# Kernel optimization log

Measured on AMD Instinct MI355X. Metric: run time of the kernel, lower is better.

## Reference

```python
import jax, jax.numpy as jnp
import numpy as np

B, S, E, H = 4, 2048, 1024, 16
HD = E // H  # 64 head dim


def setup_inputs() -> dict:
    key = jax.random.key(0)
    ks = jax.random.split(key, 6)
    x = jax.random.normal(ks[0], (B, S, E), dtype=jnp.float32)
    mask = jax.random.randint(ks[1], (B, S, S), 0, 2, dtype=jnp.int32)
    # per-head qkv Linear(E -> 3*HD), stacked over heads: weight [H, 3*HD, E]
    lim = 1.0 / np.sqrt(E)
    Wqkv = jax.random.uniform(ks[2], (H, 3 * HD, E), minval=-lim, maxval=lim, dtype=jnp.float32)
    bqkv = jax.random.uniform(ks[3], (H, 3 * HD), minval=-lim, maxval=lim, dtype=jnp.float32)
    Wo = jax.random.uniform(ks[4], (E, E), minval=-lim, maxval=lim, dtype=jnp.float32)
    bo = jax.random.uniform(ks[5], (E,), minval=-lim, maxval=lim, dtype=jnp.float32)
    return {"x": x, "mask": mask, "Wqkv": Wqkv, "bqkv": bqkv, "Wo": Wo, "bo": bo}


def reference(x, mask, Wqkv, bqkv, Wo, bo):
    # fused per-head qkv projection: [B,S,E] x [H,3HD,E] -> [B,H,S,3HD]
    qkv = jnp.einsum('bse,hfe->bhsf', x, Wqkv) + bqkv[None, :, None, :]
    q, k, v = jnp.split(qkv, 3, axis=-1)  # each [B,H,S,HD]
    scale = 1.0 / jnp.sqrt(jnp.float32(HD))
    scores = jnp.einsum('bhqd,bhkd->bhqk', q, k) * scale  # [B,H,S,S]
    # NOTE: original masked_fill sets masked scores to 0.0 (not -inf)
    scores = jnp.where(mask[:, None, :, :] == 1, 0.0, scores)
    attn = jax.nn.softmax(scores, axis=-1)
    ctx = jnp.einsum('bhqk,bhkd->bhqd', attn, v)  # [B,H,S,HD]
    ctx = ctx.transpose(0, 2, 1, 3).reshape(B, S, E)  # concat heads
    return ctx @ Wo.T + bo
```

## Files before the change

kernel.cpp:

```cpp
#include <hip/hip_runtime.h>
#include <stdint.h>

#define B_ 4
#define S_ 2048
#define E_ 1024
#define H_ 16
#define HD_ 64

typedef __attribute__((ext_vector_type(8))) short bf16x8;
typedef __attribute__((ext_vector_type(4))) float f32x4;

__device__ __forceinline__ ushort f2b(float f) {
    union { float f; uint32_t u; } c; c.f = f;
    return (ushort)((c.u + 0x8000u) >> 16);
}

__device__ __forceinline__ uint32_t pkbf(float a, float b) {
    union { float f; uint32_t u; } ca, cb; ca.f = a; cb.f = b;
#if __has_builtin(__builtin_amdgcn_perm)
    return __builtin_amdgcn_perm(cb.u + 0x8000u, ca.u + 0x8000u, 0x07060302u);
#else
    return (uint32_t)f2b(a) | ((uint32_t)f2b(b) << 16);
#endif
}

#if __has_builtin(__builtin_amdgcn_exp2f)
#define EXP2(x) __builtin_amdgcn_exp2f(x)
#else
#define EXP2(x) exp2f(x)
#endif

__device__ __forceinline__ void gl2lds16(const ushort* g, const ushort* l) {
    __builtin_amdgcn_global_load_lds(
        (const __attribute__((address_space(1))) unsigned int*)g,
        (__attribute__((address_space(3))) unsigned int*)l,
        16, 0, 0);
}

__global__ __launch_bounds__(256) void cvt_all(
    const float* __restrict__ x, const float* __restrict__ wq, const float* __restrict__ wo,
    ushort* __restrict__ xb, ushort* __restrict__ wqb, ushort* __restrict__ wob) {
    int i = blockIdx.x * 256 + threadIdx.x;
    const float* src; ushort* dst; int off;
    if (i < 2097152)      { src = x;  dst = xb;  off = i; }
    else if (i < 2883584) { src = wq; dst = wqb; off = i - 2097152; }
    else                  { src = wo; dst = wob; off = i - 2883584; }
    float4 f = ((const float4*)src)[off];
    ushort4 o;
    o.x = f2b(f.x); o.y = f2b(f.y); o.z = f2b(f.z); o.w = f2b(f.w);
    ((ushort4*)dst)[off] = o;
}

__global__ __launch_bounds__(256) void pack_mask(const int* __restrict__ mask,
                                                 uint32_t* __restrict__ mb) {
    int i = blockIdx.x * 256 + threadIdx.x;
    unsigned long long bal = __ballot(mask[i] == 1);
    int lane = threadIdx.x & 63;
    if (lane < 2) {
        int b = i >> 22, q = (i >> 11) & 2047, c = i & 2047;
        int kt = c >> 6;
        mb[((uint64_t)(b * 32 + kt) * 2048 + q) * 2 + lane] =
            (lane == 0) ? (uint32_t)bal : (uint32_t)(bal >> 32);
    }
}

template <int KD>
__device__ __forceinline__ void gemm_bt_core(
    const ushort* __restrict__ A, const ushort* __restrict__ Bm,
    int m0, int n0, ushort* As, ushort* Bs, f32x4 (&acc)[4][4])
{
    const int tid  = threadIdx.x;
    const int lane = tid & 63;
    const int wave = tid >> 6;
    const int wm = wave >> 1, wn = wave & 1;
    const int fr = lane & 15;
    const int fk = (lane >> 4) * 8;
    const int lrow = lane >> 2;
    const int lk   = (lane & 3) * 8;

    const f32x4 fz = {0.f, 0.f, 0.f, 0.f};
#pragma unroll
    for (int i = 0; i < 4; ++i)
#pragma unroll
        for (int j = 0; j < 4; ++j) acc[i][j] = fz;

    for (int kt = 0; kt < KD / 32; ++kt) {
        const int k0 = kt * 32;
        __syncthreads();
#pragma unroll
        for (int t = 0; t < 2; ++t) {
            const int r0 = t * 64 + wave * 16;
            gl2lds16(&A [(uint64_t)(m0 + r0 + lrow) * KD + k0 + lk], &As[r0 * 32]);
            gl2lds16(&Bm[(uint64_t)(n0 + r0 + lrow) * KD + k0 + lk], &Bs[r0 * 32]);
        }
        __syncthreads();
        bf16x8 af[4], bfr[4];
#pragma unroll
        for (int i = 0; i < 4; ++i)
            af[i] = *(const bf16x8*)&As[(wm * 64 + i * 16 + fr) * 32 + fk];
#pragma unroll
        for (int j = 0; j < 4; ++j)
            bfr[j] = *(const bf16x8*)&Bs[(wn * 64 + j * 16 + fr) * 32 + fk];
#pragma unroll
        for (int i = 0; i < 4; ++i)
#pragma unroll
            for (int j = 0; j < 4; ++j)
                acc[i][j] = __builtin_amdgcn_mfma_f32_16x16x32_bf16(af[i], bfr[j], acc[i][j], 0, 0, 0);
    }
}

__global__ __launch_bounds__(256) void qkv_gemm(
    const ushort* __restrict__ xb, const ushort* __restrict__ wb,
    const float* __restrict__ bqkv,
    ushort* __restrict__ qo, ushort* __restrict__ ko, ushort* __restrict__ vto)
{
    __shared__ ushort As[128 * 32];
    __shared__ ushort Bs[128 * 32];
    f32x4 acc[4][4];
    const int m0 = blockIdx.x * 128;
    const int n0 = blockIdx.y * 128;
    gemm_bt_core<1024>(xb, wb, m0, n0, As, Bs, acc);

    const int lane = threadIdx.x & 63, wave = threadIdx.x >> 6;
    const int wm = wave >> 1, wn = wave & 1;
    const int col = lane & 15, rg = lane >> 4;
    const float QSC = 0.125f * 1.4426950408889634f;
#pragma unroll
    for (int j = 0; j < 4; ++j) {
        const int n = n0 + wn * 64 + j * 16 + col;
        const int h = n / 192, f = n % 192;
        const float bias = bqkv[n];
#pragma unroll
        for (int i2 = 0; i2 < 4; ++i2) {
            const int mbase = m0 + wm * 64 + i2 * 16 + rg * 4;
            if (f < 128) {
#pragma unroll
                for (int v = 0; v < 4; ++v) {
                    const int m = mbase + v;
                    const int b = m >> 11, s = m & 2047;
                    const float val = acc[i2][j][v] + bias;
                    if (f < 64) qo[((uint64_t)(b * 16 + h) * 2048 + s) * 64 + f]        = f2b(val * QSC);
                    else        ko[((uint64_t)(b * 16 + h) * 2048 + s) * 64 + (f - 64)] = f2b(val);
                }
            } else {
                const int b = mbase >> 11, s = mbase & 2047;
                ushort4 pk;
                pk.x = f2b(acc[i2][j][0] + bias);
                pk.y = f2b(acc[i2][j][1] + bias);
                pk.z = f2b(acc[i2][j][2] + bias);
                pk.w = f2b(acc[i2][j][3] + bias);
                *(ushort4*)&vto[((uint64_t)(b * 16 + h) * 64 + (f - 128)) * 2048 + s] = pk;
            }
        }
    }
}

__global__ __launch_bounds__(256, 4) void attn_kernel(
    const ushort* __restrict__ qa, const ushort* __restrict__ ka,
    const ushort* __restrict__ vta, const uint32_t* __restrict__ mbits,
    ushort* __restrict__ ctxo)
{
    __shared__ __align__(16) ushort LDSH[16384];
    ushort* const Ks0 = LDSH;
    ushort* const Vt0 = LDSH + 4096;
    ushort* const Ks1 = LDSH + 8192;
    ushort* const Vt1 = LDSH + 12288;
    ushort* const CTX = LDSH + 8192;

    const int bid = blockIdx.x;
    const int bh = (bid & 7) * 8 + (bid >> 7);
    const int qb = (bid >> 3) & 15;
    const int b = bh >> 4;
    const int tid = threadIdx.x, lane = tid & 63, wave = tid >> 6;
    const int col = lane & 15, rg = lane >> 4;

    const uint64_t bhoff = (uint64_t)bh * (S_ * 64);
    const ushort* qp = qa + bhoff + (uint64_t)qb * 128 * 64;
    const ushort* kp = ka + bhoff;
    const ushort* vp = vta + bhoff;
    const uint32_t* mk0 = mbits + ((uint64_t)(b * 32) * 2048 + qb * 128 + wave * 32 + col) * 2;
    const uint32_t* mk1 = mk0 + 32;

    const int lr = lane >> 3;
    const int usw = (lane & 7) ^ lr;
    const int r0s = wave * 16 + lr;
    const int r1s = r0s + 8;
    const int sg0 = (r0s & 32) | ((r0s & 12) << 1) | ((r0s & 16) >> 2) | (r0s & 3);
    const int sg1 = (r1s & 32) | ((r1s & 12) << 1) | ((r1s & 16) >> 2) | (r1s & 3);
    const int kb0 = sg0 * 64 + usw * 8;
    const int kb1 = sg1 * 64 + usw * 8;
    const int vb0 = r0s * 2048 + usw * 8;
    const int vb1 = r1s * 2048 + usw * 8;
    const int ldst0 = wave * 1024;
    const int ldst1 = ldst0 + 512;

    bf16x8 aq[2][2];
#pragma unroll
    for (int i = 0; i < 2; ++i)
#pragma unroll
        for (int k2 = 0; k2 < 2; ++k2)
            aq[i][k2] = *(const bf16x8*)&qp[(wave * 32 + i * 16 + col) * 64 + k2 * 32 + rg * 8];

    gl2lds16(&kp[kb0], &Ks0[ldst0]);
    gl2lds16(&kp[kb1], &Ks0[ldst1]);
    gl2lds16(&vp[vb0], &Vt0[ldst0]);
    gl2lds16(&vp[vb1], &Vt0[ldst1]);
    uint2 mc0 = *(const uint2*)mk0;
    uint2 mc1 = *(const uint2*)mk1;
    uint2 mn0 = mc0, mn1 = mc1;
    __syncthreads();

    const f32x4 fz = {0.f, 0.f, 0.f, 0.f};
    f32x4 acc[4][2];
#pragma unroll
    for (int dt = 0; dt < 4; ++dt)
#pragma unroll
        for (int i = 0; i < 2; ++i) acc[dt][i] = fz;
    f32x4 acc5[2] = {fz, fz};

    bf16x8 vone;
#pragma unroll
    for (int e = 0; e < 8; ++e) vone[e] = (short)0x3F80;

    uint32_t bsel[2][4];
#pragma unroll
    for (int p = 0; p < 2; ++p)
#pragma unroll
        for (int v = 0; v < 4; ++v) bsel[p][v] = 1u << (rg * 8 + p * 4 + v);

    const int u0 = (rg ^ (col & 7)) << 3;

#pragma unroll 2
    for (int kt = 0; kt < 32; ++kt) {
        const int buf = kt & 1;
        const ushort* const Ksb = buf ? Ks1 : Ks0;
        const ushort* const Vtb = buf ? Vt1 : Vt0;
        ushort* const Ksn = buf ? Ks0 : Ks1;
        ushort* const Vtn = buf ? Vt0 : Vt1;

        if (kt < 31) {
            const int knext = (kt + 1) * 4096;
            gl2lds16(&kp[knext + kb0], &Ksn[ldst0]);
            gl2lds16(&kp[knext + kb1], &Ksn[ldst1]);
            gl2lds16(&vp[vb0 + (kt + 1) * 64], &Vtn[ldst0]);
            gl2lds16(&vp[vb1 + (kt + 1) * 64], &Vtn[ldst1]);
            mn0 = *(const uint2*)(mk0 + (uint64_t)(kt + 1) * 4096);
            mn1 = *(const uint2*)(mk1 + (uint64_t)(kt + 1) * 4096);
        }

        f32x4 sc[2][4];
        __builtin_amdgcn_s_setprio(1);
#pragma unroll
        for (int j = 0; j < 4; ++j) {
            bf16x8 bk0 = *(const bf16x8*)&Ksb[(j * 16 + col) * 64 + u0];
            bf16x8 bk1 = *(const bf16x8*)&Ksb[(j * 16 + col) * 64 + (u0 ^ 32)];
#pragma unroll
            for (int i = 0; i < 2; ++i) {
                f32x4 z = __builtin_amdgcn_mfma_f32_16x16x32_bf16(bk0, aq[i][0], fz, 0, 0, 0);
                sc[i][j] = __builtin_amdgcn_mfma_f32_16x16x32_bf16(bk1, aq[i][1], z, 0, 0, 0);
            }
        }
        __builtin_amdgcn_s_setprio(0);

        bf16x8 bp[2][2];
#pragma unroll
        for (int i = 0; i < 2; ++i) {
            const uint2 mw = i ? mc1 : mc0;
            union { uint32_t w[4]; bf16x8 v; } p0, p1;
#pragma unroll
            for (int j = 0; j < 4; ++j) {
                const uint32_t w = (j & 2) ? mw.y : mw.x;
                const int p = j & 1;
                float pe[4];
#pragma unroll
                for (int v = 0; v < 4; ++v) {
                    const float s = (w & bsel[p][v]) ? 0.f : sc[i][j][v];
                    pe[v] = EXP2(s);
                }
                const uint32_t lo = pkbf(pe[0], pe[1]);
                const uint32_t hi = pkbf(pe[2], pe[3]);
                if (j < 2) { p0.w[p * 2] = lo; p0.w[p * 2 + 1] = hi; }
                else       { p1.w[p * 2] = lo; p1.w[p * 2 + 1] = hi; }
            }
            bp[i][0] = p0.v;
            bp[i][1] = p1.v;
        }

        __builtin_amdgcn_s_setprio(1);
#pragma unroll
        for (int i = 0; i < 2; ++i) {
            acc5[i] = __builtin_amdgcn_mfma_f32_16x16x32_bf16(vone, bp[i][0], acc5[i], 0, 0, 0);
            acc5[i] = __builtin_amdgcn_mfma_f32_16x16x32_bf16(vone, bp[i][1], acc5[i], 0, 0, 0);
        }
#pragma unroll
        for (int dt = 0; dt < 4; ++dt) {
            bf16x8 av0 = *(const bf16x8*)&Vtb[(dt * 16 + col) * 64 + u0];
            bf16x8 av1 = *(const bf16x8*)&Vtb[(dt * 16 + col) * 64 + (u0 ^ 32)];
#pragma unroll
            for (int i = 0; i < 2; ++i) {
                acc[dt][i] = __builtin_amdgcn_mfma_f32_16x16x32_bf16(av0, bp[i][0], acc[dt][i], 0, 0, 0);
                acc[dt][i] = __builtin_amdgcn_mfma_f32_16x16x32_bf16(av1, bp[i][1], acc[dt][i], 0, 0, 0);
            }
        }
        __builtin_amdgcn_s_setprio(0);
        __syncthreads();
        mc0 = mn0; mc1 = mn1;
    }

    float linv[2];
#pragma unroll
    for (int i = 0; i < 2; ++i) linv[i] = 1.0f / acc5[i][0];

#pragma unroll
    for (int dt = 0; dt < 4; ++dt)
#pragma unroll
        for (int i = 0; i < 2; ++i) {
            const int q = wave * 32 + i * 16 + col;
            const int d = dt * 16 + rg * 4;
            const int gg = (d >> 3) ^ (q & 7);
            ushort4 pk;
            pk.x = f2b(acc[dt][i][0] * linv[i]);
            pk.y = f2b(acc[dt][i][1] * linv[i]);
            pk.z = f2b(acc[dt][i][2] * linv[i]);
            pk.w = f2b(acc[dt][i][3] * linv[i]);
            *(ushort4*)&CTX[q * 64 + gg * 8 + (d & 7)] = pk;
        }
    __syncthreads();
    const int h = bh & 15;
    const uint64_t obase = (uint64_t)(b * S_ + qb * 128) * E_ + (uint64_t)h * 64;
#pragma unroll
    for (int t4 = 0; t4 < 4; ++t4) {
        const int id = tid + t4 * 256;
        const int r = id >> 3, c8 = id & 7;
        *(bf16x8*)&ctxo[obase + (uint64_t)r * E_ + c8 * 8] =
            *(const bf16x8*)&CTX[r * 64 + ((c8 ^ (r & 7)) << 3)];
    }
}

__global__ __launch_bounds__(256) void out_gemm(
    const ushort* __restrict__ ctxb, const ushort* __restrict__ wob,
    const float* __restrict__ bo, float* __restrict__ out)
{
    __shared__ ushort As[128 * 32];
    __shared__ ushort Bs[128 * 32];
    f32x4 acc[4][4];
    const int m0 = blockIdx.x * 128;
    const int n0 = blockIdx.y * 128;
    gemm_bt_core<1024>(ctxb, wob, m0, n0, As, Bs, acc);

    const int lane = threadIdx.x & 63, wave = threadIdx.x >> 6;
    const int wm = wave >> 1, wn = wave & 1;
    const int col = lane & 15, rg = lane >> 4;
#pragma unroll
    for (int j = 0; j < 4; ++j) {
        const int n = n0 + wn * 64 + j * 16 + col;
        const float bias = bo[n];
#pragma unroll
        for (int i2 = 0; i2 < 4; ++i2) {
            const int mb2 = m0 + wm * 64 + i2 * 16 + rg * 4;
#pragma unroll
            for (int v = 0; v < 4; ++v)
                out[(uint64_t)(mb2 + v) * 1024 + n] = acc[i2][j][v] + bias;
        }
    }
}

extern "C" void kernel_launch(void* const* d_in, const int* in_sizes, int n_in,
                              void* d_out, int out_size, void* d_ws, size_t ws_size,
                              hipStream_t stream)
{
    const float* x    = (const float*)d_in[0];
    const int*   mask = (const int*)d_in[1];
    const float* Wqkv = (const float*)d_in[2];
    const float* bqkv = (const float*)d_in[3];
    const float* Wo   = (const float*)d_in[4];
    const float* bo   = (const float*)d_in[5];
    float* out = (float*)d_out;

    char* p = (char*)d_ws;
    ushort* xb  = (ushort*)p; p += (size_t)8388608 * 2;
    ushort* wqb = (ushort*)p; p += (size_t)3145728 * 2;
    ushort* wob = (ushort*)p; p += (size_t)1048576 * 2;
    ushort* qo  = (ushort*)p; p += (size_t)8388608 * 2;
    ushort* ko  = (ushort*)p; p += (size_t)8388608 * 2;
    ushort* vto = (ushort*)p; p += (size_t)8388608 * 2;
    ushort* ctx = (ushort*)p; p += (size_t)8388608 * 2;
    uint32_t* mb = (uint32_t*)p;

    cvt_all<<<12288, 256, 0, stream>>>(x, Wqkv, Wo, xb, wqb, wob);
    pack_mask<<<65536, 256, 0, stream>>>(mask, mb);
    qkv_gemm<<<dim3(64, 24), 256, 0, stream>>>(xb, wqb, bqkv, qo, ko, vto);
    attn_kernel<<<1024, 256, 0, stream>>>(qo, ko, vto, mb, ctx);
    out_gemm<<<dim3(64, 8), 256, 0, stream>>>(ctx, wob, bo, out);
}
```

Before: 374.6 us.

## Triple-buffer K/V tiles in attention kernel with prefetch distance two

Switches the attention kernel's K/V LDS staging from double to triple buffering. Loads are issued two tiles ahead, and a partial vmcnt wait lets the next tile's loads stay in flight across the barrier, which is meant to hide more global-to-LDS latency. The cost is 50% more LDS per block and launch bounds lowered from 4 to 3 blocks per CU, so occupancy may drop. It also relies on manual waitcnt counts, which must match the number of outstanding loads exactly.

```diff
diff --git a/kernel.cpp b/kernel.cpp
--- a/kernel.cpp
+++ b/kernel.cpp
@@ -155,17 +155,19 @@
     }
 }
 
-__global__ __launch_bounds__(256, 4) void attn_kernel(
+__global__ __launch_bounds__(256, 3) void attn_kernel(
     const ushort* __restrict__ qa, const ushort* __restrict__ ka,
     const ushort* __restrict__ vta, const uint32_t* __restrict__ mbits,
     ushort* __restrict__ ctxo)
 {
-    __shared__ __align__(16) ushort LDSH[16384];
+    __shared__ __align__(16) ushort LDSH[24576];
     ushort* const Ks0 = LDSH;
     ushort* const Vt0 = LDSH + 4096;
     ushort* const Ks1 = LDSH + 8192;
     ushort* const Vt1 = LDSH + 12288;
-    ushort* const CTX = LDSH + 8192;
+    ushort* const Ks2 = LDSH + 16384;
+    ushort* const Vt2 = LDSH + 20480;
+    ushort* const CTX = LDSH;
 
     const int bid = blockIdx.x;
     const int bh = (bid & 7) * 8 + (bid >> 7);
@@ -205,10 +207,18 @@
     gl2lds16(&kp[kb1], &Ks0[ldst1]);
     gl2lds16(&vp[vb0], &Vt0[ldst0]);
     gl2lds16(&vp[vb1], &Vt0[ldst1]);
-    uint2 mc0 = *(const uint2*)mk0;
-    uint2 mc1 = *(const uint2*)mk1;
-    uint2 mn0 = mc0, mn1 = mc1;
-    __syncthreads();
+    uint2 m_cur0 = *(const uint2*)mk0;
+    uint2 m_cur1 = *(const uint2*)mk1;
+    gl2lds16(&kp[4096 + kb0], &Ks1[ldst0]);
+    gl2lds16(&kp[4096 + kb1], &Ks1[ldst1]);
+    gl2lds16(&vp[vb0 + 64], &Vt1[ldst0]);
+    gl2lds16(&vp[vb1 + 64], &Vt1[ldst1]);
+    uint2 m_nxt0 = *(const uint2*)(mk0 + 4096);
+    uint2 m_nxt1 = *(const uint2*)(mk1 + 4096);
+    uint2 m_new0 = m_nxt0, m_new1 = m_nxt1;
+    asm volatile("s_waitcnt vmcnt(0)" ::: "memory");
+    __builtin_amdgcn_s_barrier();
+    __builtin_amdgcn_sched_barrier(0);
 
     const f32x4 fz = {0.f, 0.f, 0.f, 0.f};
     f32x4 acc[4][2];
@@ -230,30 +240,27 @@
 
     const int u0 = (rg ^ (col & 7)) << 3;
 
-#pragma unroll 2
+    const ushort* cK = Ks0; const ushort* cV = Vt0;
+    const ushort* nK = Ks1; const ushort* nV = Vt1;
+    ushort* tK = Ks2; ushort* tV = Vt2;
+
     for (int kt = 0; kt < 32; ++kt) {
-        const int buf = kt & 1;
-        const ushort* const Ksb = buf ? Ks1 : Ks0;
-        const ushort* const Vtb = buf ? Vt1 : Vt0;
-        ushort* const Ksn = buf ? Ks0 : Ks1;
-        ushort* const Vtn = buf ? Vt0 : Vt1;
-
-        if (kt < 31) {
-            const int knext = (kt + 1) * 4096;
-            gl2lds16(&kp[knext + kb0], &Ksn[ldst0]);
-            gl2lds16(&kp[knext + kb1], &Ksn[ldst1]);
-            gl2lds16(&vp[vb0 + (kt + 1) * 64], &Vtn[ldst0]);
-            gl2lds16(&vp[vb1 + (kt + 1) * 64], &Vtn[ldst1]);
-            mn0 = *(const uint2*)(mk0 + (uint64_t)(kt + 1) * 4096);
-            mn1 = *(const uint2*)(mk1 + (uint64_t)(kt + 1) * 4096);
+        if (kt < 30) {
+            const int k2 = (kt + 2) * 4096;
+            gl2lds16(&kp[k2 + kb0], &tK[ldst0]);
+            gl2lds16(&kp[k2 + kb1], &tK[ldst1]);
+            gl2lds16(&vp[vb0 + (kt + 2) * 64], &tV[ldst0]);
+            gl2lds16(&vp[vb1 + (kt + 2) * 64], &tV[ldst1]);
+            m_new0 = *(const uint2*)(mk0 + (uint64_t)(kt + 2) * 4096);
+            m_new1 = *(const uint2*)(mk1 + (uint64_t)(kt + 2) * 4096);
         }
 
         f32x4 sc[2][4];
         __builtin_amdgcn_s_setprio(1);
 #pragma unroll
         for (int j = 0; j < 4; ++j) {
-            bf16x8 bk0 = *(const bf16x8*)&Ksb[(j * 16 + col) * 64 + u0];
-            bf16x8 bk1 = *(const bf16x8*)&Ksb[(j * 16 + col) * 64 + (u0 ^ 32)];
+            bf16x8 bk0 = *(const bf16x8*)&cK[(j * 16 + col) * 64 + u0];
+            bf16x8 bk1 = *(const bf16x8*)&cK[(j * 16 + col) * 64 + (u0 ^ 32)];
 #pragma unroll
             for (int i = 0; i < 2; ++i) {
                 f32x4 z = __builtin_amdgcn_mfma_f32_16x16x32_bf16(bk0, aq[i][0], fz, 0, 0, 0);
@@ -265,7 +272,7 @@
         bf16x8 bp[2][2];
 #pragma unroll
         for (int i = 0; i < 2; ++i) {
-            const uint2 mw = i ? mc1 : mc0;
+            const uint2 mw = i ? m_cur1 : m_cur0;
             union { uint32_t w[4]; bf16x8 v; } p0, p1;
 #pragma unroll
             for (int j = 0; j < 4; ++j) {
@@ -294,8 +301,8 @@
         }
 #pragma unroll
         for (int dt = 0; dt < 4; ++dt) {
-            bf16x8 av0 = *(const bf16x8*)&Vtb[(dt * 16 + col) * 64 + u0];
-            bf16x8 av1 = *(const bf16x8*)&Vtb[(dt * 16 + col) * 64 + (u0 ^ 32)];
+            bf16x8 av0 = *(const bf16x8*)&cV[(dt * 16 + col) * 64 + u0];
+            bf16x8 av1 = *(const bf16x8*)&cV[(dt * 16 + col) * 64 + (u0 ^ 32)];
 #pragma unroll
             for (int i = 0; i < 2; ++i) {
                 acc[dt][i] = __builtin_amdgcn_mfma_f32_16x16x32_bf16(av0, bp[i][0], acc[dt][i], 0, 0, 0);
@@ -303,8 +310,18 @@
             }
         }
         __builtin_amdgcn_s_setprio(0);
-        __syncthreads();
-        mc0 = mn0; mc1 = mn1;
+
+        if (kt < 30) {
+            asm volatile("s_waitcnt vmcnt(6)" ::: "memory");
+        } else {
+            asm volatile("s_waitcnt vmcnt(0)" ::: "memory");
+        }
+        __builtin_amdgcn_s_barrier();
+        __builtin_amdgcn_sched_barrier(0);
+
+        const ushort* oK = cK; const ushort* oV = cV;
+        cK = nK; cV = nV; nK = tK; nV = tV; tK = (ushort*)oK; tV = (ushort*)oV;
+        m_cur0 = m_nxt0; m_cur1 = m_nxt1; m_nxt0 = m_new0; m_nxt1 = m_new1;
     }
 
     float linv[2];
```

Measured after the change: 361.0 us. 1.04x faster.
